# Optimization experiments

Measured on AMD Instinct MI355X. Metric: run time of the kernel, lower is better.

The kernel has to match this reference:

```python
import jax, jax.numpy as jnp
import numpy as np

N, E, F, H, C, G = 100000, 800000, 128, 128, 10, 128
EPS = 1e-5


def setup_inputs() -> dict:
    key = jax.random.key(0)
    ks = jax.random.split(key, 8)
    return {
        "x": jax.random.normal(ks[0], (N, F), jnp.float32),
        "edge_index": jax.random.randint(ks[1], (2, E), 0, N),
        "batch": jnp.sort(jax.random.randint(ks[2], (N,), 0, G)),
        "edge_weight": jax.random.uniform(ks[3], (E,), jnp.float32, 0.1, 1.0),
        "bn_feat_w": jnp.ones((F,), jnp.float32),
        "bn_feat_b": jnp.full((F,), 1e-4, jnp.float32),
        "conv_feat_W": jax.random.normal(ks[4], (F, H), jnp.float32) / np.float32(np.sqrt(F)),
        "conv_feat_b": jnp.zeros((H,), jnp.float32),
        "bns_w": jnp.ones((3, H), jnp.float32),
        "bns_b": jnp.full((3, H), 1e-4, jnp.float32),
        "convs_W": jax.random.normal(ks[5], (3, H, H), jnp.float32) / np.float32(np.sqrt(H)),
        "convs_b": jnp.zeros((3, H), jnp.float32),
        "bn_fc_w": jnp.ones((H,), jnp.float32),
        "bn_fc_b": jnp.full((H,), 1e-4, jnp.float32),
        "lin_fc_W": jax.random.normal(ks[6], (H, H), jnp.float32) / np.float32(np.sqrt(H)),
        "lin_fc_b": jnp.zeros((H,), jnp.float32),
        "bn_hidden_w": jnp.ones((H,), jnp.float32),
        "bn_hidden_b": jnp.full((H,), 1e-4, jnp.float32),
        "lin_class_W": jax.random.normal(ks[7], (H, C), jnp.float32) / np.float32(np.sqrt(H)),
        "lin_class_b": jnp.zeros((C,), jnp.float32),
    }


def _bn(h, w, b):
    # training-mode BatchNorm1d: biased batch stats over dim 0
    mu = h.mean(0)
    var = jnp.mean((h - mu) ** 2, 0)
    return (h - mu) * jax.lax.rsqrt(var + EPS) * w + b


def reference(x, edge_index, batch, edge_weight,
              bn_feat_w, bn_feat_b, conv_feat_W, conv_feat_b,
              bns_w, bns_b, convs_W, convs_b,
              bn_fc_w, bn_fc_b, lin_fc_W, lin_fc_b,
              bn_hidden_w, bn_hidden_b, lin_class_W, lin_class_b):
    n = x.shape[0]
    loops = jnp.arange(n)
    # PyG GCNConv: add self-loops (weight 1) + symmetric normalization, shared by all convs
    row = jnp.concatenate([edge_index[0], loops])
    col = jnp.concatenate([edge_index[1], loops])
    ew = jnp.concatenate([edge_weight, jnp.ones((n,), x.dtype)])
    deg = jax.ops.segment_sum(ew, col, num_segments=n)
    dinv = jnp.where(deg > 0, jax.lax.rsqrt(jnp.maximum(deg, EPS)), 0.0)
    norm = (dinv[row] * ew * dinv[col])[:, None]  # [E+N, 1]

    def conv(h, W, b):
        m = (h @ W)[row] * norm                 # gather + scale per edge
        return jax.ops.segment_sum(m, col, num_segments=n) + b

    h = _bn(x, bn_feat_w, bn_feat_b)
    h = jax.nn.relu(conv(h, conv_feat_W, conv_feat_b))
    h_init = h

    x_list = []
    # branch 1: BN -> Conv -> ReLU chain
    h = h_init
    for i in range(3):
        h = jax.nn.relu(conv(_bn(h, bns_w[i], bns_b[i]), convs_W[i], convs_b[i]))
    x_list.append(h)
    # branch 2: double application of the same BN/Conv per step
    h = h_init
    for i in range(3):
        h_ = jax.nn.relu(conv(_bn(h, bns_w[i], bns_b[i]), convs_W[i], convs_b[i]))
        h = jax.nn.relu(conv(_bn(h_, bns_w[i], bns_b[i]), convs_W[i], convs_b[i]))
    x_list.append(h)
    # branch 3: identical to branch 1 when conv_residual=False
    h = h_init
    for i in range(3):
        h = jax.nn.relu(conv(_bn(h, bns_w[i], bns_b[i]), convs_W[i], convs_b[i]))
    x_list.append(h)
    # branch 4: BN -> ReLU only
    h = h_init
    for i in range(3):
        h = jax.nn.relu(_bn(h, bns_w[i], bns_b[i]))
    x_list.append(h)

    def head(hn):
        g = jax.ops.segment_sum(hn, batch, num_segments=G)  # global_add_pool
        g = jax.nn.relu(_bn(g, bn_fc_w, bn_fc_b) @ lin_fc_W + lin_fc_b)
        g = _bn(g, bn_hidden_w, bn_hidden_b)
        return jax.nn.log_softmax(g @ lin_class_W + lin_class_b, axis=-1)

    return tuple(head(hn) for hn in x_list)
```

## Files before the change

kernel.cpp:

```cpp
#include <hip/hip_runtime.h>

#define N_NODES 100000
#define NPAD    100032
#define NBLK    1563
#define NEDGE   800000
#define NGRP    128
#define NSLOT   32
#define EPS     1e-5f

typedef unsigned int   u32;
typedef unsigned short u16;
typedef short bf16x8 __attribute__((ext_vector_type(8)));
typedef float f32x4  __attribute__((ext_vector_type(4)));

__device__ __forceinline__ float bf2f(u32 u){ return __uint_as_float(u << 16); }
__device__ __forceinline__ u16 f2bf(float f){
  u32 x = __float_as_uint(f);
  x += 0x7fffu + ((x >> 16) & 1u);
  return (u16)(x >> 16);
}

__global__ void k_init(float* deg, int* cnt, int* fill, float* gbuf){
  int i = blockIdx.x * 256 + threadIdx.x;
  if (i < NPAD){ deg[i] = 1.0f; cnt[i] = 0; fill[i] = 0; }
  if (i < 4 * NGRP * 128) gbuf[i] = 0.f;
}

__global__ void k_deg(const int* __restrict__ col, const float* __restrict__ ew,
                      float* __restrict__ deg, int* __restrict__ cnt){
  int e = blockIdx.x * 256 + threadIdx.x;
  if (e < NEDGE){
    int c = col[e];
    atomicAdd(&deg[c], ew[e]);
    atomicAdd(&cnt[c], 1);
  }
}

__global__ void k_dinv(const float* __restrict__ deg, float* __restrict__ dinv, float* __restrict__ srow){
  int i = blockIdx.x * 256 + threadIdx.x;
  if (i < N_NODES){
    float d = deg[i];
    float v = d > 0.f ? rsqrtf(fmaxf(d, EPS)) : 0.f;
    dinv[i] = v; srow[i] = v * v;
  }
}

__global__ __launch_bounds__(256) void k_chunksum(const int* __restrict__ cnt, int* __restrict__ csum){
  int b = blockIdx.x, t = threadIdx.x;
  int s = 0;
  for (int i = t; i < 1024; i += 256){ int idx = b * 1024 + i; if (idx < N_NODES) s += cnt[idx]; }
  __shared__ int red[256];
  red[t] = s; __syncthreads();
  for (int o = 128; o > 0; o >>= 1){ if (t < o) red[t] += red[t + o]; __syncthreads(); }
  if (t == 0) csum[b] = red[0];
}

__global__ __launch_bounds__(128) void k_chunkscan(const int* __restrict__ csum, int* __restrict__ coff,
                                                   int* __restrict__ ptrA){
  int t = threadIdx.x;
  __shared__ int s[128];
  int v = (t < 98) ? csum[t] : 0;
  s[t] = v; __syncthreads();
  for (int o = 1; o < 128; o <<= 1){
    int x = (t >= o) ? s[t - o] : 0;
    __syncthreads(); s[t] += x; __syncthreads();
  }
  if (t < 98) coff[t] = s[t] - v;
  if (t == 0) ptrA[N_NODES] = NEDGE;
}

__global__ __launch_bounds__(256) void k_scan2(const int* __restrict__ cnt, const int* __restrict__ coff,
                                               int* __restrict__ ptrA){
  int b = blockIdx.x, t = threadIdx.x;
  int base = b * 1024 + t * 4;
  int v[4], tot = 0;
  #pragma unroll
  for (int k = 0; k < 4; k++){ int idx = base + k; v[k] = (idx < N_NODES) ? cnt[idx] : 0; tot += v[k]; }
  __shared__ int sc[256];
  sc[t] = tot; __syncthreads();
  for (int o = 1; o < 256; o <<= 1){
    int x = (t >= o) ? sc[t - o] : 0;
    __syncthreads(); sc[t] += x; __syncthreads();
  }
  int off = coff[b] + sc[t] - tot;
  #pragma unroll
  for (int k = 0; k < 4; k++){ int idx = base + k; if (idx < N_NODES) ptrA[idx] = off; off += v[k]; }
}

__global__ void k_fill(const int* __restrict__ row, const int* __restrict__ col,
                       const float* __restrict__ ew, const float* __restrict__ dinv,
                       const int* __restrict__ ptrA, int* __restrict__ fill, int2* __restrict__ adj,
                       float* __restrict__ srow){
  int e = blockIdx.x * 256 + threadIdx.x;
  if (e < NEDGE){
    int r = row[e], c = col[e];
    float w = dinv[r] * ew[e] * dinv[c];
    int pos = ptrA[c] + atomicAdd(&fill[c], 1);
    adj[pos] = make_int2(r, __float_as_int(w));
    atomicAdd(&srow[c], w);
  }
}

__global__ __launch_bounds__(256) void k_bhist(const int* __restrict__ batch, int* __restrict__ bpart){
  __shared__ int loc[128];
  int t = threadIdx.x;
  if (t < 128) loc[t] = 0;
  __syncthreads();
  int i = blockIdx.x * 256 + t;
  if (i < N_NODES) atomicAdd(&loc[batch[i]], 1);
  __syncthreads();
  if (t < 128) bpart[blockIdx.x * 128 + t] = loc[t];
}

__global__ __launch_bounds__(128) void k_bscan(const int* __restrict__ bpart, int* __restrict__ gptr){
  int t = threadIdx.x;
  int v = 0;
  for (int p = 0; p < 391; p++) v += bpart[p * 128 + t];
  __shared__ int s[128];
  s[t] = v; __syncthreads();
  for (int o = 1; o < 128; o <<= 1){
    int x = (t >= o) ? s[t - o] : 0;
    __syncthreads(); s[t] += x; __syncthreads();
  }
  gptr[t + 1] = s[t];
  if (t == 0) gptr[0] = 0;
}

__global__ __launch_bounds__(256) void k_cvtstats(const float* __restrict__ x, u32* __restrict__ dst,
                                                  float* __restrict__ sums_out){
  __shared__ float R[1024];
  int t = threadIdx.x;
  float s0 = 0.f, q0 = 0.f, s1 = 0.f, q1 = 0.f;
  size_t base = (size_t)blockIdx.x * 4096 + t;
  #pragma unroll
  for (int it = 0; it < 16; it++){
    size_t idx = base + (size_t)it * 256;
    if (idx < (size_t)N_NODES * 64){
      float2 v = ((const float2*)x)[idx];
      dst[idx] = (u32)f2bf(v.x) | ((u32)f2bf(v.y) << 16);
      s0 += v.x; q0 += v.x * v.x; s1 += v.y; q1 += v.y * v.y;
    }
  }
  R[t] = s0; R[256 + t] = q0; R[512 + t] = s1; R[768 + t] = q1;
  __syncthreads();
  if (t < 64){
    float S0 = 0.f, Q0 = 0.f, S1 = 0.f, Q1 = 0.f;
    #pragma unroll
    for (int g = 0; g < 4; g++){
      S0 += R[g * 64 + t];       Q0 += R[256 + g * 64 + t];
      S1 += R[512 + g * 64 + t]; Q1 += R[768 + g * 64 + t];
    }
    float* so = sums_out + (blockIdx.x & (NSLOT - 1)) * 256;
    atomicAdd(&so[2 * t], S0);
    atomicAdd(&so[2 * t + 1], S1);
    atomicAdd(&so[128 + 2 * t], Q0);
    atomicAdd(&so[128 + 2 * t + 1], Q1);
  }
}

__global__ __launch_bounds__(1024) void k_fold(const float* __restrict__ sums,
    const float* __restrict__ bw, const float* __restrict__ bb,
    const float* __restrict__ W, const float* __restrict__ bias,
    u16* __restrict__ Wh, u16* __restrict__ Wl, float* __restrict__ rb){
  __shared__ float scl[128], shf[128], rbs[128], stot[256];
  int t = threadIdx.x;
  if (t < 256){
    float s = 0.f;
    #pragma unroll 4
    for (int sl = 0; sl < NSLOT; sl++) s += sums[sl * 256 + t];
    stot[t] = s;
  } else if (t < 384) rbs[t - 256] = 0.f;
  __syncthreads();
  if (t < 128){
    float mu  = stot[t] * (1.f / N_NODES);
    float var = stot[128 + t] * (1.f / N_NODES) - mu * mu;
    float sc  = bw[t] * rsqrtf(var + EPS);
    scl[t] = sc; shf[t] = bb[t] - mu * sc;
  }
  __syncthreads();
  #pragma unroll
  for (int r = 0; r < 2; r++){
    int idx = r * 1024 + t;
    int lane_ = idx & 63, sl = idx >> 6;
    int nt_ = sl >> 2, ks_ = sl & 3;
    int n_ = nt_ * 16 + (lane_ & 15);
    int kb = ks_ * 32 + (lane_ >> 4) * 8;
    float rp = 0.f;
    u16 hi8[8], lo8[8];
    #pragma unroll
    for (int j = 0; j < 8; j++){
      float wv = W[(kb + j) * 128 + n_];
      rp += shf[kb + j] * wv;
      float xv = scl[kb + j] * wv;
      u16 hh = f2bf(xv);
      hi8[j] = hh; lo8[j] = f2bf(xv - bf2f(hh));
    }
    uint4 ph, pl;
    ph.x = (u32)hi8[0] | ((u32)hi8[1] << 16); ph.y = (u32)hi8[2] | ((u32)hi8[3] << 16);
    ph.z = (u32)hi8[4] | ((u32)hi8[5] << 16); ph.w = (u32)hi8[6] | ((u32)hi8[7] << 16);
    pl.x = (u32)lo8[0] | ((u32)lo8[1] << 16); pl.y = (u32)lo8[2] | ((u32)lo8[3] << 16);
    pl.z = (u32)lo8[4] | ((u32)lo8[5] << 16); pl.w = (u32)lo8[6] | ((u32)lo8[7] << 16);
    *(uint4*)&Wh[idx * 8] = ph;
    *(uint4*)&Wl[idx * 8] = pl;
    atomicAdd(&rbs[n_], rp);
  }
  __syncthreads();
  if (t < 128){
    rb[t] = rbs[t];
    rb[128 + t] = bias[t];
  }
}

#define CONV_EPILOGUE(RB, HOUT, SOUT)                                          \
  __syncthreads();                                                             \
  sred[t] = 0.f;                                                               \
  __syncthreads();                                                             \
  _Pragma("unroll")                                                            \
  for (int nt = 0; nt < 8; nt++){                                              \
    int colc = nt * 16 + m;                                                    \
    float rv = RB[colc], bv = RB[128 + colc];                                  \
    float s = 0.f, qq = 0.f;                                                   \
    _Pragma("unroll")                                                          \
    for (int r = 0; r < 4; r++){                                               \
      int rown = row0 + q * 4 + r;                                             \
      float v = C[nt][r] + srow[rown] * rv + bv;                               \
      v = fmaxf(v, 0.f);                                                       \
      u16 sv = f2bf(v);                                                        \
      HOUT[(size_t)rown * 128 + colc] = sv;                                    \
      if (rown < N_NODES){ float vv = bf2f(sv); s += vv; qq += vv * vv; }      \
    }                                                                          \
    atomicAdd(&sred[colc], s);                                                 \
    atomicAdd(&sred[128 + colc], qq);                                          \
  }                                                                            \
  __syncthreads();                                                             \
  atomicAdd(&SOUT[(blockIdx.x & (NSLOT - 1)) * 256 + t], sred[t]);

#define GATHER_PHASE()                                                         \
  _Pragma("unroll")                                                            \
  for (int ks = 0; ks < 4; ks++)                                               \
    _Pragma("unroll")                                                          \
    for (int j = 0; j < 8; j++) acc[ks][j] = 0.f;                              \
  if (i < N_NODES){                                                            \
    const u16* hq = h + q * 8;                                                 \
    float di = dinv[i], sw = di * di;                                          \
    _Pragma("unroll")                                                          \
    for (int ks = 0; ks < 4; ks++){                                            \
      uint4 v = *(const uint4*)(hq + (size_t)i * 128 + ks * 32);               \
      acc[ks][0] = sw * __uint_as_float(v.x << 16); acc[ks][1] = sw * __uint_as_float(v.x & 0xffff0000u); \
      acc[ks][2] = sw * __uint_as_float(v.y << 16); acc[ks][3] = sw * __uint_as_float(v.y & 0xffff0000u); \
      acc[ks][4] = sw * __uint_as_float(v.z << 16); acc[ks][5] = sw * __uint_as_float(v.z & 0xffff0000u); \
      acc[ks][6] = sw * __uint_as_float(v.w << 16); acc[ks][7] = sw * __uint_as_float(v.w & 0xffff0000u); \
    }                                                                          \
    int b = ptrA[i], e = ptrA[i + 1];                                          \
    int k = b;                                                                 \
    for (; k + 2 <= e; k += 2){                                                \
      int2 a0 = adj[k], a1 = adj[k + 1];                                       \
      const u16* r0p = hq + (size_t)a0.x * 128;                                \
      const u16* r1p = hq + (size_t)a1.x * 128;                                \
      uint4 u0 = *(const uint4*)(r0p);                                         \
      uint4 u1 = *(const uint4*)(r0p + 32);                                    \
      uint4 u2 = *(const uint4*)(r0p + 64);                                    \
      uint4 u3 = *(const uint4*)(r0p + 96);                                    \
      uint4 w0 = *(const uint4*)(r1p);                                         \
      uint4 w1 = *(const uint4*)(r1p + 32);                                    \
      uint4 w2 = *(const uint4*)(r1p + 64);                                    \
      uint4 w3 = *(const uint4*)(r1p + 96);                                    \
      float f0 = __int_as_float(a0.y), f1 = __int_as_float(a1.y);              \
      FMA_KS(0, u0, f0) FMA_KS(1, u1, f0) FMA_KS(2, u2, f0) FMA_KS(3, u3, f0)  \
      FMA_KS(0, w0, f1) FMA_KS(1, w1, f1) FMA_KS(2, w2, f1) FMA_KS(3, w3, f1)  \
    }                                                                          \
    for (; k < e; k++){                                                        \
      int2 a0 = adj[k];                                                        \
      const u16* r0p = hq + (size_t)a0.x * 128;                                \
      uint4 u0 = *(const uint4*)(r0p);                                         \
      uint4 u1 = *(const uint4*)(r0p + 32);                                    \
      uint4 u2 = *(const uint4*)(r0p + 64);                                    \
      uint4 u3 = *(const uint4*)(r0p + 96);                                    \
      float f0 = __int_as_float(a0.y);                                         \
      FMA_KS(0, u0, f0) FMA_KS(1, u1, f0) FMA_KS(2, u2, f0) FMA_KS(3, u3, f0)  \
    }                                                                          \
  }

#define FMA_KS(KS, V, WT) \
  acc[KS][0] += (WT) * __uint_as_float((V).x << 16); acc[KS][1] += (WT) * __uint_as_float((V).x & 0xffff0000u); \
  acc[KS][2] += (WT) * __uint_as_float((V).y << 16); acc[KS][3] += (WT) * __uint_as_float((V).y & 0xffff0000u); \
  acc[KS][4] += (WT) * __uint_as_float((V).z << 16); acc[KS][5] += (WT) * __uint_as_float((V).z & 0xffff0000u); \
  acc[KS][6] += (WT) * __uint_as_float((V).w << 16); acc[KS][7] += (WT) * __uint_as_float((V).w & 0xffff0000u);

#define MFMA_3PASS(WH, WL_)                                                    \
  _Pragma("unroll")                                                            \
  for (int ks = 0; ks < 4; ks++){                                              \
    _Pragma("unroll")                                                          \
    for (int nt = 0; nt < 8; nt++){                                            \
      bf16x8 bh = ((const bf16x8*)WH)[(nt * 4 + ks) * 64 + lane];              \
      bf16x8 bl = ((const bf16x8*)WL_)[(nt * 4 + ks) * 64 + lane];             \
      C[nt] = __builtin_amdgcn_mfma_f32_16x16x32_bf16(AH[ks], bh, C[nt], 0, 0, 0); \
      C[nt] = __builtin_amdgcn_mfma_f32_16x16x32_bf16(AL[ks], bh, C[nt], 0, 0, 0); \
      C[nt] = __builtin_amdgcn_mfma_f32_16x16x32_bf16(AH[ks], bl, C[nt], 0, 0, 0); \
    }                                                                          \
  }

__global__ __launch_bounds__(256, 4) void k_conv(
    const u16* __restrict__ h, const int* __restrict__ ptrA, const int2* __restrict__ adj,
    const float* __restrict__ dinv, const float* __restrict__ srow,
    const u16* __restrict__ Wh, const u16* __restrict__ Wl, const float* __restrict__ rb,
    u16* __restrict__ hout, float* __restrict__ sums_out){
  __shared__ float sred[256];
  int t = threadIdx.x;
  int wave = t >> 6, lane = t & 63, m = lane & 15, q = lane >> 4;
  int row0 = blockIdx.x * 64 + wave * 16;
  int i = row0 + m;
  float acc[4][8];
  GATHER_PHASE()
  bf16x8 AH[4], AL[4];
  #pragma unroll
  for (int ks = 0; ks < 4; ks++)
    #pragma unroll
    for (int j = 0; j < 8; j++){
      u16 hh = f2bf(acc[ks][j]);
      AH[ks][j] = (short)hh;
      AL[ks][j] = (short)f2bf(acc[ks][j] - bf2f(hh));
    }
  f32x4 C[8];
  #pragma unroll
  for (int nt = 0; nt < 8; nt++) C[nt] = f32x4{0.f, 0.f, 0.f, 0.f};
  MFMA_3PASS(Wh, Wl)
  CONV_EPILOGUE(rb, hout, sums_out)
}

__global__ __launch_bounds__(256, 4) void k_dualconv(
    const u16* __restrict__ h, const int* __restrict__ ptrA, const int2* __restrict__ adj,
    const float* __restrict__ dinv, const float* __restrict__ srow,
    const u16* __restrict__ Wh1, const u16* __restrict__ Wl1, const float* __restrict__ rb1,
    u16* __restrict__ hout1, float* __restrict__ sums1,
    const u16* __restrict__ Wh2, const u16* __restrict__ Wl2, const float* __restrict__ rb2,
    u16* __restrict__ hout2, float* __restrict__ sums2){
  __shared__ float sred[256];
  int t = threadIdx.x;
  int wave = t >> 6, lane = t & 63, m = lane & 15, q = lane >> 4;
  int row0 = blockIdx.x * 64 + wave * 16;
  int i = row0 + m;
  float acc[4][8];
  GATHER_PHASE()
  bf16x8 AH[4], AL[4];
  #pragma unroll
  for (int ks = 0; ks < 4; ks++)
    #pragma unroll
    for (int j = 0; j < 8; j++){
      u16 hh = f2bf(acc[ks][j]);
      AH[ks][j] = (short)hh;
      AL[ks][j] = (short)f2bf(acc[ks][j] - bf2f(hh));
    }
  f32x4 C[8];
  #pragma unroll
  for (int nt = 0; nt < 8; nt++) C[nt] = f32x4{0.f, 0.f, 0.f, 0.f};
  MFMA_3PASS(Wh1, Wl1)
  CONV_EPILOGUE(rb1, hout1, sums1)
  #pragma unroll
  for (int nt = 0; nt < 8; nt++) C[nt] = f32x4{0.f, 0.f, 0.f, 0.f};
  MFMA_3PASS(Wh2, Wl2)
  CONV_EPILOGUE(rb2, hout2, sums2)
}

__global__ __launch_bounds__(256) void k_normrelu(const u16* __restrict__ h, const float* __restrict__ sums,
    const float* __restrict__ bw, const float* __restrict__ bb, u16* __restrict__ o,
    float* __restrict__ sums_out){
  __shared__ float scl[128], shf[128], R[1024], stot[256];
  int t = threadIdx.x;
  {
    float s = 0.f;
    #pragma unroll 4
    for (int sl = 0; sl < NSLOT; sl++) s += sums[sl * 256 + t];
    stot[t] = s;
  }
  __syncthreads();
  if (t < 128){
    float mu  = stot[t] * (1.f / N_NODES);
    float var = stot[128 + t] * (1.f / N_NODES) - mu * mu;
    float sc  = bw[t] * rsqrtf(var + EPS);
    scl[t] = sc; shf[t] = bb[t] - mu * sc;
  }
  __syncthreads();
  int c0 = (t & 63) * 2;
  float sc0 = scl[c0], sh0 = shf[c0], sc1 = scl[c0 + 1], sh1 = shf[c0 + 1];
  float s0 = 0.f, q0 = 0.f, s1 = 0.f, q1 = 0.f;
  size_t base = (size_t)blockIdx.x * 4096 + t;
  #pragma unroll
  for (int it = 0; it < 16; it++){
    size_t idx = base + (size_t)it * 256;
    if (idx < (size_t)N_NODES * 64){
      u32 v = ((const u32*)h)[idx];
      float x0 = fmaxf(bf2f(v & 0xffffu) * sc0 + sh0, 0.f);
      float x1 = fmaxf(bf2f(v >> 16) * sc1 + sh1, 0.f);
      u16 r0 = f2bf(x0), r1 = f2bf(x1);
      ((u32*)o)[idx] = (u32)r0 | ((u32)r1 << 16);
      float y0 = bf2f(r0), y1 = bf2f(r1);
      s0 += y0; q0 += y0 * y0; s1 += y1; q1 += y1 * y1;
    }
  }
  R[t] = s0; R[256 + t] = q0; R[512 + t] = s1; R[768 + t] = q1;
  __syncthreads();
  if (t < 64){
    float S0 = 0.f, Q0 = 0.f, S1 = 0.f, Q1 = 0.f;
    #pragma unroll
    for (int g = 0; g < 4; g++){
      S0 += R[g * 64 + t];       Q0 += R[256 + g * 64 + t];
      S1 += R[512 + g * 64 + t]; Q1 += R[768 + g * 64 + t];
    }
    float* so = sums_out + (blockIdx.x & (NSLOT - 1)) * 256;
    atomicAdd(&so[2 * t], S0);
    atomicAdd(&so[2 * t + 1], S1);
    atomicAdd(&so[128 + 2 * t], Q0);
    atomicAdd(&so[128 + 2 * t + 1], Q1);
  }
}

__global__ __launch_bounds__(128) void k_pool(const u16* __restrict__ h, const int* __restrict__ gptr,
                                              float* __restrict__ gdst){
  int g = blockIdx.x >> 3, s = blockIdx.x & 7, t = threadIdx.x;
  int b = gptr[g], e = gptr[g + 1];
  int len = e - b, per = (len + 7) >> 3;
  int r0 = b + s * per, r1 = min(r0 + per, e);
  float acc = 0.f;
  for (int r = r0; r < r1; r++) acc += bf2f(h[(size_t)r * 128 + t]);
  atomicAdd(&gdst[g * 128 + t], acc);
}

__global__ __launch_bounds__(256) void k_head(const float* __restrict__ gbuf,
    const float* __restrict__ fcw, const float* __restrict__ fcb,
    const float* __restrict__ Wfc, const float* __restrict__ bfc,
    const float* __restrict__ bhw, const float* __restrict__ bhb,
    const float* __restrict__ Wcl, const float* __restrict__ bcl,
    float* __restrict__ out){
  __shared__ float GS[128 * 65];
  __shared__ float ls[256], lq[256];
  __shared__ float scl[128], shf[128], scl2[128], shf2[128];
  __shared__ float sumT[128], sumQ[128];
  __shared__ float WclT[1280], Lrow[1280];
  int t = threadIdx.x, br = blockIdx.x;
  int slot = (br == 1) ? 1 : (br == 3 ? 3 : 0);
  const float* G = gbuf + slot * 16384;
  {
    int col = t & 127, hf2 = t >> 7;
    float s = 0.f, q = 0.f;
    for (int g = hf2 * 64; g < hf2 * 64 + 64; g++){ float v = G[g * 128 + col]; s += v; q += v * v; }
    ls[t] = s; lq[t] = q;
  }
  for (int idx = t; idx < 1280; idx += 256){
    int cc = idx >> 7, c = idx & 127;
    WclT[idx] = Wcl[c * 10 + cc];
  }
  if (t < 128){ sumT[t] = 0.f; sumQ[t] = 0.f; }
  __syncthreads();
  if (t < 128){
    float s = ls[t] + ls[t + 128], q = lq[t] + lq[t + 128];
    float mu = s * (1.f / 128), var = q * (1.f / 128) - mu * mu;
    float sc = fcw[t] * rsqrtf(var + EPS);
    scl[t] = sc; shf[t] = fcb[t] - mu * sc;
  }
  __syncthreads();
  int tr = t >> 4, tc = t & 15, r0 = tr * 8, c0 = tc * 8;
  float acc[8][8];
  #pragma unroll
  for (int a = 0; a < 8; a++)
    #pragma unroll
    for (int b = 0; b < 8; b++) acc[a][b] = 0.f;
  for (int kh = 0; kh < 2; kh++){
    for (int idx = t; idx < 8192; idx += 256){
      int r = idx >> 6, kk = idx & 63, f = kh * 64 + kk;
      GS[r * 65 + kk] = G[r * 128 + f] * scl[f] + shf[f];
    }
    __syncthreads();
    #pragma unroll 2
    for (int k = 0; k < 64; k++){
      float a[8];
      #pragma unroll
      for (int ri = 0; ri < 8; ri++) a[ri] = GS[(r0 + ri) * 65 + k];
      float4 b0 = *(const float4*)&Wfc[(kh * 64 + k) * 128 + c0];
      float4 b1 = *(const float4*)&Wfc[(kh * 64 + k) * 128 + c0 + 4];
      float bb[8] = {b0.x, b0.y, b0.z, b0.w, b1.x, b1.y, b1.z, b1.w};
      #pragma unroll
      for (int ri = 0; ri < 8; ri++)
        #pragma unroll
        for (int ci = 0; ci < 8; ci++) acc[ri][ci] += a[ri] * bb[ci];
    }
    __syncthreads();
  }
  #pragma unroll
  for (int ci = 0; ci < 8; ci++){
    float bb = bfc[c0 + ci];
    float s = 0.f, q = 0.f;
    #pragma unroll
    for (int ri = 0; ri < 8; ri++){
      float v = fmaxf(acc[ri][ci] + bb, 0.f);
      acc[ri][ci] = v; s += v; q += v * v;
    }
    atomicAdd(&sumT[c0 + ci], s);
    atomicAdd(&sumQ[c0 + ci], q);
  }
  __syncthreads();
  if (t < 128){
    float mu = sumT[t] * (1.f / 128), var = sumQ[t] * (1.f / 128) - mu * mu;
    float sc = bhw[t] * rsqrtf(var + EPS);
    scl2[t] = sc; shf2[t] = bhb[t] - mu * sc;
  }
  __syncthreads();
  #pragma unroll
  for (int ci = 0; ci < 8; ci++){
    float sc = scl2[c0 + ci], sh = shf2[c0 + ci];
    #pragma unroll
    for (int ri = 0; ri < 8; ri++) acc[ri][ci] = acc[ri][ci] * sc + sh;
  }
  #pragma unroll
  for (int ri = 0; ri < 8; ri++){
    float pl[10];
    #pragma unroll
    for (int cc = 0; cc < 10; cc++) pl[cc] = 0.f;
    #pragma unroll
    for (int ci = 0; ci < 8; ci++){
      float v = acc[ri][ci];
      #pragma unroll
      for (int cc = 0; cc < 10; cc++) pl[cc] += v * WclT[cc * 128 + c0 + ci];
    }
    #pragma unroll
    for (int msk = 1; msk < 16; msk <<= 1)
      #pragma unroll
      for (int cc = 0; cc < 10; cc++) pl[cc] += __shfl_xor(pl[cc], msk, 64);
    if (tc == 0)
      #pragma unroll
      for (int cc = 0; cc < 10; cc++) Lrow[(r0 + ri) * 10 + cc] = pl[cc];
  }
  __syncthreads();
  if (t < 128){
    float l[10];
    #pragma unroll
    for (int cc = 0; cc < 10; cc++) l[cc] = Lrow[t * 10 + cc] + bcl[cc];
    float m = l[0];
    #pragma unroll
    for (int cc = 1; cc < 10; cc++) m = fmaxf(m, l[cc]);
    float se = 0.f;
    #pragma unroll
    for (int cc = 0; cc < 10; cc++) se += expf(l[cc] - m);
    float lse = m + logf(se);
    #pragma unroll
    for (int cc = 0; cc < 10; cc++) out[br * 1280 + t * 10 + cc] = l[cc] - lse;
  }
}

extern "C" void kernel_launch(void* const* d_in, const int* in_sizes, int n_in,
                              void* d_out, int out_size, void* d_ws, size_t ws_size,
                              hipStream_t stream){
  const float* x    = (const float*)d_in[0];
  const int*  ei    = (const int*)d_in[1];
  const int*  batch = (const int*)d_in[2];
  const float* ew   = (const float*)d_in[3];
  const float* bnfw = (const float*)d_in[4];
  const float* bnfb = (const float*)d_in[5];
  const float* cfW  = (const float*)d_in[6];
  const float* cfb  = (const float*)d_in[7];
  const float* bnsw = (const float*)d_in[8];
  const float* bnsb = (const float*)d_in[9];
  const float* cvW  = (const float*)d_in[10];
  const float* cvb  = (const float*)d_in[11];
  const float* fcw  = (const float*)d_in[12];
  const float* fcb  = (const float*)d_in[13];
  const float* Wfc  = (const float*)d_in[14];
  const float* bfc  = (const float*)d_in[15];
  const float* bhw  = (const float*)d_in[16];
  const float* bhb  = (const float*)d_in[17];
  const float* Wcl  = (const float*)d_in[18];
  const float* bcl  = (const float*)d_in[19];
  float* out = (float*)d_out;

  char* p = (char*)d_ws;
  auto carve = [&](size_t bytes)->void*{ void* r = (void*)p; p += (bytes + 255) & ~(size_t)255; return r; };
  float* deg  = (float*)carve((size_t)NPAD * 4);
  float* dinv = (float*)carve((size_t)NPAD * 4);
  float* srow = (float*)carve((size_t)NPAD * 4);
  int*   cnt  = (int*)carve((size_t)NPAD * 4);
  int*   fill = (int*)carve((size_t)NPAD * 4);
  int*   ptrA = (int*)carve((size_t)(NPAD + 1) * 4);
  int*   bpart= (int*)carve((size_t)391 * 128 * 4);
  int*   csum = (int*)carve(512);
  int*   coff = (int*)carve(512);
  int*   gptr = (int*)carve(1024);
  float* S    = (float*)carve((size_t)13 * NSLOT * 1024);
  float* gbuf = (float*)carve(4 * 128 * 128 * 4);
  u16*   F0h  = (u16*)carve(32768);  u16* F0l = (u16*)carve(32768);  float* F0r = (float*)carve(1024);
  u16*   F1h  = (u16*)carve(32768);  u16* F1l = (u16*)carve(32768);  float* F1r = (float*)carve(1024);
  u16*   F2h  = (u16*)carve(32768);  u16* F2l = (u16*)carve(32768);  float* F2r = (float*)carve(1024);
  u16*   B0   = (u16*)carve((size_t)NPAD * 256);
  u16*   B1   = (u16*)carve((size_t)NPAD * 256);
  u16*   B2   = (u16*)carve((size_t)NPAD * 256);
  u16*   B3   = (u16*)carve((size_t)NPAD * 256);
  int2*  adj  = (int2*)carve((size_t)NEDGE * 8);
  u16*   Xb   = B3;
  auto Sb = [&](int i){ return S + (size_t)i * NSLOT * 256; };

  (void)hipMemsetAsync(S, 0, (size_t)13 * NSLOT * 1024, stream);

  k_init<<<392, 256, 0, stream>>>(deg, cnt, fill, gbuf);
  k_deg<<<3125, 256, 0, stream>>>(ei + NEDGE, ew, deg, cnt);
  k_dinv<<<391, 256, 0, stream>>>(deg, dinv, srow);
  k_chunksum<<<98, 256, 0, stream>>>(cnt, csum);
  k_chunkscan<<<1, 128, 0, stream>>>(csum, coff, ptrA);
  k_scan2<<<98, 256, 0, stream>>>(cnt, coff, ptrA);
  k_fill<<<3125, 256, 0, stream>>>(ei, ei + NEDGE, ew, dinv, ptrA, fill, adj, srow);
  k_bhist<<<391, 256, 0, stream>>>(batch, bpart);
  k_bscan<<<1, 128, 0, stream>>>(bpart, gptr);
  k_cvtstats<<<NBLK, 256, 0, stream>>>(x, (u32*)Xb, Sb(0));

  auto fold = [&](const float* Sin, const float* bw, const float* bb,
                  const float* W, const float* bias, u16* Fh, u16* Fl, float* Fr){
    k_fold<<<1, 1024, 0, stream>>>(Sin, bw, bb, W, bias, Fh, Fl, Fr);
  };
  auto conv = [&](const u16* hin, const u16* Fh, const u16* Fl, const float* Fr,
                  u16* hout, float* Sout){
    k_conv<<<NBLK, 256, 0, stream>>>(hin, ptrA, adj, dinv, srow, Fh, Fl, Fr, hout, Sout);
  };

  fold(Sb(0), bnfw, bnfb, cfW, cfb, F0h, F0l, F0r);
  conv(Xb, F0h, F0l, F0r, B0, Sb(1));
  fold(Sb(1), bnsw, bnsb, cvW, cvb, F1h, F1l, F1r);
  conv(B0, F1h, F1l, F1r, B1, Sb(2));
  k_normrelu<<<NBLK, 256, 0, stream>>>(B0, Sb(1), bnsw,       bnsb,       B2, Sb(3));
  k_normrelu<<<NBLK, 256, 0, stream>>>(B2, Sb(3), bnsw + 128, bnsb + 128, B3, Sb(4));
  k_normrelu<<<NBLK, 256, 0, stream>>>(B3, Sb(4), bnsw + 256, bnsb + 256, B2, Sb(12));
  k_pool<<<1024, 128, 0, stream>>>(B2, gptr, gbuf + 3 * 16384);
  fold(Sb(2), bnsw + 128, bnsb + 128, cvW + 16384, cvb + 128, F0h, F0l, F0r);
  fold(Sb(2), bnsw,       bnsb,       cvW,         cvb,       F1h, F1l, F1r);
  k_dualconv<<<NBLK, 256, 0, stream>>>(B1, ptrA, adj, dinv, srow,
      F0h, F0l, F0r, B3, Sb(5),
      F1h, F1l, F1r, B2, Sb(6));
  fold(Sb(5), bnsw + 256, bnsb + 256, cvW + 32768, cvb + 256, F2h, F2l, F2r);
  conv(B3, F2h, F2l, F2r, B0, Sb(10));
  k_pool<<<1024, 128, 0, stream>>>(B0, gptr, gbuf);
  fold(Sb(6), bnsw + 128, bnsb + 128, cvW + 16384, cvb + 128, F0h, F0l, F0r);
  conv(B2, F0h, F0l, F0r, B1, Sb(7));
  fold(Sb(7), bnsw + 128, bnsb + 128, cvW + 16384, cvb + 128, F1h, F1l, F1r);
  conv(B1, F1h, F1l, F1r, B2, Sb(8));
  fold(Sb(8), bnsw + 256, bnsb + 256, cvW + 32768, cvb + 256, F2h, F2l, F2r);
  conv(B2, F2h, F2l, F2r, B1, Sb(9));
  fold(Sb(9), bnsw + 256, bnsb + 256, cvW + 32768, cvb + 256, F0h, F0l, F0r);
  conv(B1, F0h, F0l, F0r, B3, Sb(11));
  k_pool<<<1024, 128, 0, stream>>>(B3, gptr, gbuf + 16384);

  k_head<<<4, 256, 0, stream>>>(gbuf, fcw, fcb, Wfc, bfc, bhw, bhb, Wcl, bcl, out);
}
```

Measured before the change: 1.197 ms.

## Sort nodes by in-degree and process heaviest blocks first in conv kernels

Builds a counting-sort permutation of nodes by in-degree (histogram, scan, scatter) and has the conv and dual-conv kernels process rows through that permutation. Each 16-row wave then gathers over neighbour lists of similar length, which cuts lane divergence in the edge loop. Blocks are launched in reverse so the high-degree rows start first, which reduces tail imbalance. The launch bounds also drop from 4 to 2 waves per SIMD, giving more registers. Costs are scattered output writes, an extra indirection per row, three small setup kernels, and possibly lower occupancy.

```diff
diff --git a/kernel.cpp b/kernel.cpp
--- a/kernel.cpp
+++ b/kernel.cpp
@@ -20,10 +20,11 @@
   return (u16)(x >> 16);
 }
 
-__global__ void k_init(float* deg, int* cnt, int* fill, float* gbuf){
+__global__ void k_init(float* deg, int* cnt, int* fill, float* gbuf, int* dh){
   int i = blockIdx.x * 256 + threadIdx.x;
   if (i < NPAD){ deg[i] = 1.0f; cnt[i] = 0; fill[i] = 0; }
   if (i < 4 * NGRP * 128) gbuf[i] = 0.f;
+  if (i < 1024) dh[i] = 0;
 }
 
 __global__ void k_deg(const int* __restrict__ col, const float* __restrict__ ew,
@@ -42,6 +43,39 @@
     float d = deg[i];
     float v = d > 0.f ? rsqrtf(fmaxf(d, EPS)) : 0.f;
     dinv[i] = v; srow[i] = v * v;
+  }
+}
+
+__global__ __launch_bounds__(256) void k_dhist(const int* __restrict__ cnt, int* __restrict__ dh){
+  __shared__ int loc[1024];
+  int t = threadIdx.x;
+  #pragma unroll
+  for (int j = t; j < 1024; j += 256) loc[j] = 0;
+  __syncthreads();
+  int i = blockIdx.x * 256 + t;
+  if (i < N_NODES) atomicAdd(&loc[min(cnt[i], 1023)], 1);
+  __syncthreads();
+  #pragma unroll
+  for (int j = t; j < 1024; j += 256) if (loc[j]) atomicAdd(&dh[j], loc[j]);
+}
+
+__global__ __launch_bounds__(1024) void k_dscan(const int* __restrict__ dh, int* __restrict__ doff){
+  __shared__ int s[1024];
+  int t = threadIdx.x;
+  int v = dh[t];
+  s[t] = v; __syncthreads();
+  for (int o = 1; o < 1024; o <<= 1){
+    int x = (t >= o) ? s[t - o] : 0;
+    __syncthreads(); s[t] += x; __syncthreads();
+  }
+  doff[t] = s[t] - v;
+}
+
+__global__ void k_dperm(const int* __restrict__ cnt, int* __restrict__ doff, int* __restrict__ perm){
+  int i = blockIdx.x * 256 + threadIdx.x;
+  if (i < N_NODES){
+    int pos = atomicAdd(&doff[min(cnt[i], 1023)], 1);
+    perm[pos] = i;
   }
 }
 
@@ -211,6 +245,16 @@
   }
 }
 
+#define PR_SETUP()                                                             \
+  int pr4[4]; float sr4[4];                                                    \
+  _Pragma("unroll")                                                            \
+  for (int r = 0; r < 4; r++){                                                 \
+    int rown = row0 + q * 4 + r;                                               \
+    int prr = (rown < N_NODES) ? perm[rown] : -1;                              \
+    pr4[r] = prr;                                                              \
+    sr4[r] = (prr >= 0) ? srow[prr] : 0.f;                                     \
+  }
+
 #define CONV_EPILOGUE(RB, HOUT, SOUT)                                          \
   __syncthreads();                                                             \
   sred[t] = 0.f;                                                               \
@@ -222,12 +266,13 @@
     float s = 0.f, qq = 0.f;                                                   \
     _Pragma("unroll")                                                          \
     for (int r = 0; r < 4; r++){                                               \
-      int rown = row0 + q * 4 + r;                                             \
-      float v = C[nt][r] + srow[rown] * rv + bv;                               \
-      v = fmaxf(v, 0.f);                                                       \
-      u16 sv = f2bf(v);                                                        \
-      HOUT[(size_t)rown * 128 + colc] = sv;                                    \
-      if (rown < N_NODES){ float vv = bf2f(sv); s += vv; qq += vv * vv; }      \
+      if (pr4[r] >= 0){                                                        \
+        float v = C[nt][r] + sr4[r] * rv + bv;                                 \
+        v = fmaxf(v, 0.f);                                                     \
+        u16 sv = f2bf(v);                                                      \
+        HOUT[(size_t)pr4[r] * 128 + colc] = sv;                                \
+        float vv = bf2f(sv); s += vv; qq += vv * vv;                           \
+      }                                                                        \
     }                                                                          \
     atomicAdd(&sred[colc], s);                                                 \
     atomicAdd(&sred[128 + colc], qq);                                          \
@@ -240,18 +285,18 @@
   for (int ks = 0; ks < 4; ks++)                                               \
     _Pragma("unroll")                                                          \
     for (int j = 0; j < 8; j++) acc[ks][j] = 0.f;                              \
-  if (i < N_NODES){                                                            \
+  if (ip >= 0){                                                                \
     const u16* hq = h + q * 8;                                                 \
-    float di = dinv[i], sw = di * di;                                          \
+    float di = dinv[ip], sw = di * di;                                         \
     _Pragma("unroll")                                                          \
     for (int ks = 0; ks < 4; ks++){                                            \
-      uint4 v = *(const uint4*)(hq + (size_t)i * 128 + ks * 32);               \
+      uint4 v = *(const uint4*)(hq + (size_t)ip * 128 + ks * 32);              \
       acc[ks][0] = sw * __uint_as_float(v.x << 16); acc[ks][1] = sw * __uint_as_float(v.x & 0xffff0000u); \
       acc[ks][2] = sw * __uint_as_float(v.y << 16); acc[ks][3] = sw * __uint_as_float(v.y & 0xffff0000u); \
       acc[ks][4] = sw * __uint_as_float(v.z << 16); acc[ks][5] = sw * __uint_as_float(v.z & 0xffff0000u); \
       acc[ks][6] = sw * __uint_as_float(v.w << 16); acc[ks][7] = sw * __uint_as_float(v.w & 0xffff0000u); \
     }                                                                          \
-    int b = ptrA[i], e = ptrA[i + 1];                                          \
+    int b = ptrA[ip], e = ptrA[ip + 1];                                        \
     int k = b;                                                                 \
     for (; k + 2 <= e; k += 2){                                                \
       int2 a0 = adj[k], a1 = adj[k + 1];                                       \
@@ -300,16 +345,18 @@
     }                                                                          \
   }
 
-__global__ __launch_bounds__(256, 4) void k_conv(
+__global__ __launch_bounds__(256, 2) void k_conv(
     const u16* __restrict__ h, const int* __restrict__ ptrA, const int2* __restrict__ adj,
-    const float* __restrict__ dinv, const float* __restrict__ srow,
+    const float* __restrict__ dinv, const float* __restrict__ srow, const int* __restrict__ perm,
     const u16* __restrict__ Wh, const u16* __restrict__ Wl, const float* __restrict__ rb,
     u16* __restrict__ hout, float* __restrict__ sums_out){
   __shared__ float sred[256];
   int t = threadIdx.x;
   int wave = t >> 6, lane = t & 63, m = lane & 15, q = lane >> 4;
-  int row0 = blockIdx.x * 64 + wave * 16;
+  int bi = gridDim.x - 1 - blockIdx.x;
+  int row0 = bi * 64 + wave * 16;
   int i = row0 + m;
+  int ip = (i < N_NODES) ? perm[i] : -1;
   float acc[4][8];
   GATHER_PHASE()
   bf16x8 AH[4], AL[4];
@@ -325,12 +372,13 @@
   #pragma unroll
   for (int nt = 0; nt < 8; nt++) C[nt] = f32x4{0.f, 0.f, 0.f, 0.f};
   MFMA_3PASS(Wh, Wl)
+  PR_SETUP()
   CONV_EPILOGUE(rb, hout, sums_out)
 }
 
-__global__ __launch_bounds__(256, 4) void k_dualconv(
+__global__ __launch_bounds__(256, 2) void k_dualconv(
     const u16* __restrict__ h, const int* __restrict__ ptrA, const int2* __restrict__ adj,
-    const float* __restrict__ dinv, const float* __restrict__ srow,
+    const float* __restrict__ dinv, const float* __restrict__ srow, const int* __restrict__ perm,
     const u16* __restrict__ Wh1, const u16* __restrict__ Wl1, const float* __restrict__ rb1,
     u16* __restrict__ hout1, float* __restrict__ sums1,
     const u16* __restrict__ Wh2, const u16* __restrict__ Wl2, const float* __restrict__ rb2,
@@ -338,8 +386,10 @@
   __shared__ float sred[256];
   int t = threadIdx.x;
   int wave = t >> 6, lane = t & 63, m = lane & 15, q = lane >> 4;
-  int row0 = blockIdx.x * 64 + wave * 16;
+  int bi = gridDim.x - 1 - blockIdx.x;
+  int row0 = bi * 64 + wave * 16;
   int i = row0 + m;
+  int ip = (i < N_NODES) ? perm[i] : -1;
   float acc[4][8];
   GATHER_PHASE()
   bf16x8 AH[4], AL[4];
@@ -355,6 +405,7 @@
   #pragma unroll
   for (int nt = 0; nt < 8; nt++) C[nt] = f32x4{0.f, 0.f, 0.f, 0.f};
   MFMA_3PASS(Wh1, Wl1)
+  PR_SETUP()
   CONV_EPILOGUE(rb1, hout1, sums1)
   #pragma unroll
   for (int nt = 0; nt < 8; nt++) C[nt] = f32x4{0.f, 0.f, 0.f, 0.f};
@@ -580,6 +631,9 @@
   int*   cnt  = (int*)carve((size_t)NPAD * 4);
   int*   fill = (int*)carve((size_t)NPAD * 4);
   int*   ptrA = (int*)carve((size_t)(NPAD + 1) * 4);
+  int*   perm = (int*)carve((size_t)NPAD * 4);
+  int*   dh   = (int*)carve(4096);
+  int*   doff = (int*)carve(4096);
   int*   bpart= (int*)carve((size_t)391 * 128 * 4);
   int*   csum = (int*)carve(512);
   int*   coff = (int*)carve(512);
@@ -599,9 +653,12 @@
 
   (void)hipMemsetAsync(S, 0, (size_t)13 * NSLOT * 1024, stream);
 
-  k_init<<<392, 256, 0, stream>>>(deg, cnt, fill, gbuf);
+  k_init<<<392, 256, 0, stream>>>(deg, cnt, fill, gbuf, dh);
   k_deg<<<3125, 256, 0, stream>>>(ei + NEDGE, ew, deg, cnt);
   k_dinv<<<391, 256, 0, stream>>>(deg, dinv, srow);
+  k_dhist<<<391, 256, 0, stream>>>(cnt, dh);
+  k_dscan<<<1, 1024, 0, stream>>>(dh, doff);
+  k_dperm<<<391, 256, 0, stream>>>(cnt, doff, perm);
   k_chunksum<<<98, 256, 0, stream>>>(cnt, csum);
   k_chunkscan<<<1, 128, 0, stream>>>(csum, coff, ptrA);
   k_scan2<<<98, 256, 0, stream>>>(cnt, coff, ptrA);
@@ -616,7 +673,7 @@
   };
   auto conv = [&](const u16* hin, const u16* Fh, const u16* Fl, const float* Fr,
                   u16* hout, float* Sout){
-    k_conv<<<NBLK, 256, 0, stream>>>(hin, ptrA, adj, dinv, srow, Fh, Fl, Fr, hout, Sout);
+    k_conv<<<NBLK, 256, 0, stream>>>(hin, ptrA, adj, dinv, srow, perm, Fh, Fl, Fr, hout, Sout);
   };
 
   fold(Sb(0), bnfw, bnfb, cfW, cfb, F0h, F0l, F0r);
@@ -629,7 +686,7 @@
   k_pool<<<1024, 128, 0, stream>>>(B2, gptr, gbuf + 3 * 16384);
   fold(Sb(2), bnsw + 128, bnsb + 128, cvW + 16384, cvb + 128, F0h, F0l, F0r);
   fold(Sb(2), bnsw,       bnsb,       cvW,         cvb,       F1h, F1l, F1r);
-  k_dualconv<<<NBLK, 256, 0, stream>>>(B1, ptrA, adj, dinv, srow,
+  k_dualconv<<<NBLK, 256, 0, stream>>>(B1, ptrA, adj, dinv, srow, perm,
       F0h, F0l, F0r, B3, Sb(5),
       F1h, F1l, F1r, B2, Sb(6));
   fold(Sb(5), bnsw + 256, bnsb + 256, cvW + 32768, cvb + 256, F2h, F2l, F2r);
```

After: 1.616 ms. +35.1%, slower.
